# Optimization experiments

Hardware: AMD Instinct MI355X
Metric: run time of the kernel (lower is better)

The kernel has to match this reference:

```python
import jax, jax.numpy as jnp
import numpy as np

NH = 16            # num_heads
HD = 64            # head_dim
HID = NH * HD      # hidden_size = 1024
MLP = 4 * HID      # mlp_hidden_dim = 4096
B, LI, LT = 1, 2048, 512
EPS = 1e-6


def _ln(x):
    # LayerNorm without affine, eps=1e-6
    mu = jnp.mean(x, -1, keepdims=True)
    var = jnp.mean((x - mu) ** 2, -1, keepdims=True)
    return (x - mu) * jax.lax.rsqrt(var + EPS)


def _rms(x, scale):
    # QK RMSNorm over head_dim with learned scale
    return x * jax.lax.rsqrt(jnp.mean(x * x, -1, keepdims=True) + EPS) * scale


def _modulate(vec, w, b):
    # Modulation(double=True): Linear(silu(vec)) -> 6 chunks, broadcast over seq
    out = jnp.dot(jax.nn.silu(vec), w) + b           # [B, 6*HID]
    return jnp.split(out[:, None, :], 6, axis=-1)


def _qkv(x_mod, qkv_w, q_scale, k_scale):
    b, l, _ = x_mod.shape
    qkv = jnp.dot(x_mod, qkv_w).reshape(b, l, 3, NH, HD)
    qkv = jnp.transpose(qkv, (2, 0, 3, 1, 4))         # [3, B, H, L, D]
    q, k, v = qkv[0], qkv[1], qkv[2]
    return _rms(q, q_scale), _rms(k, k_scale), v


def _attn(q, k, v):
    s = jnp.einsum('bhqd,bhkd->bhqk', q, k) * (HD ** -0.5)
    a = jax.nn.softmax(s, axis=-1)
    o = jnp.einsum('bhqk,bhkd->bhqd', a, v)
    b, h, l, d = o.shape
    return jnp.transpose(o, (0, 2, 1, 3)).reshape(b, l, h * d)  # B L (H D)


def _mlp(x, w1, b1, w2, b2):
    return jnp.dot(jax.nn.gelu(jnp.dot(x, w1) + b1, approximate=True), w2) + b2


def setup_inputs() -> dict:
    key = jax.random.key(0)
    ks = iter(jax.random.split(key, 40))
    def rn(shape, s=1.0):
        return jax.random.normal(next(ks), shape, jnp.float32) * s
    return {
        'img': rn((B, LI, HID)),
        'txt': rn((B, LT, HID)),
        'vec': rn((B, HID)),
        'img_mod_w': rn((HID, 6 * HID), 0.02), 'img_mod_b': jnp.zeros((6 * HID,), jnp.float32),
        'txt_mod_w': rn((HID, 6 * HID), 0.02), 'txt_mod_b': jnp.zeros((6 * HID,), jnp.float32),
        'img_qkv_w': rn((HID, 3 * HID), 0.02),
        'img_q_scale': jnp.ones((HD,), jnp.float32), 'img_k_scale': jnp.ones((HD,), jnp.float32),
        'img_proj_w': rn((HID, HID), 0.02), 'img_proj_b': jnp.zeros((HID,), jnp.float32),
        'img_mlp_w1': rn((HID, MLP), 0.02), 'img_mlp_b1': jnp.zeros((MLP,), jnp.float32),
        'img_mlp_w2': rn((MLP, HID), 0.02), 'img_mlp_b2': jnp.zeros((HID,), jnp.float32),
        'txt_qkv_w': rn((HID, 3 * HID), 0.02),
        'txt_q_scale': jnp.ones((HD,), jnp.float32), 'txt_k_scale': jnp.ones((HD,), jnp.float32),
        'txt_proj_w': rn((HID, HID), 0.02), 'txt_proj_b': jnp.zeros((HID,), jnp.float32),
        'txt_mlp_w1': rn((HID, MLP), 0.02), 'txt_mlp_b1': jnp.zeros((MLP,), jnp.float32),
        'txt_mlp_w2': rn((MLP, HID), 0.02), 'txt_mlp_b2': jnp.zeros((HID,), jnp.float32),
    }


def reference(img, txt, vec,
              img_mod_w, img_mod_b, txt_mod_w, txt_mod_b,
              img_qkv_w, img_q_scale, img_k_scale, img_proj_w, img_proj_b,
              img_mlp_w1, img_mlp_b1, img_mlp_w2, img_mlp_b2,
              txt_qkv_w, txt_q_scale, txt_k_scale, txt_proj_w, txt_proj_b,
              txt_mlp_w1, txt_mlp_b1, txt_mlp_w2, txt_mlp_b2):
    i_sh1, i_sc1, i_g1, i_sh2, i_sc2, i_g2 = _modulate(vec, img_mod_w, img_mod_b)
    t_sh1, t_sc1, t_g1, t_sh2, t_sc2, t_g2 = _modulate(vec, txt_mod_w, txt_mod_b)
    iq, ik, iv = _qkv((1 + i_sc1) * _ln(img) + i_sh1, img_qkv_w, img_q_scale, img_k_scale)
    tq, tk, tv = _qkv((1 + t_sc1) * _ln(txt) + t_sh1, txt_qkv_w, txt_q_scale, txt_k_scale)
    q = jnp.concatenate((tq, iq), axis=2)   # txt tokens first, as in source
    k = jnp.concatenate((tk, ik), axis=2)
    v = jnp.concatenate((tv, iv), axis=2)
    attn = _attn(q, k, v)                    # [B, LT+LI, HID]
    lt = txt.shape[1]
    txt_a, img_a = attn[:, :lt], attn[:, lt:]
    img = img + i_g1 * (jnp.dot(img_a, img_proj_w) + img_proj_b)
    img = img + i_g2 * _mlp((1 + i_sc2) * _ln(img) + i_sh2, img_mlp_w1, img_mlp_b1, img_mlp_w2, img_mlp_b2)
    txt = txt + t_g1 * (jnp.dot(txt_a, txt_proj_w) + txt_proj_b)
    txt = txt + t_g2 * _mlp((1 + t_sc2) * _ln(txt) + t_sh2, txt_mlp_w1, txt_mlp_b1, txt_mlp_w2, txt_mlp_b2)
    return (img, txt)
```

## Files before the change

kernel.cpp:

```cpp
#include <hip/hip_runtime.h>
#include <hip/hip_bf16.h>
#include <stdint.h>


#define NHEAD 16
#define HDIM  64
#define HIDD  1024
#define MLPD  4096
#define L_IMG 2048
#define L_TXT 512
#define L_TOT 2560
#define EPSV  1e-6f
#define LOG2E 1.44269504088896f

typedef __attribute__((ext_vector_type(8))) __bf16 bf16x8;
typedef __attribute__((ext_vector_type(4))) float  f32x4;

__device__ __forceinline__ float u2f(uint16_t u) {
    uint32_t i = (uint32_t)u << 16;
    float f; __builtin_memcpy(&f, &i, 4);
    return f;
}
__device__ __forceinline__ uint16_t f2u(float f) {
    uint32_t i; __builtin_memcpy(&i, &f, 4);
    uint32_t r = (i + 0x7fffu + ((i >> 16) & 1u)) >> 16;
    return (uint16_t)r;
}
__device__ __forceinline__ uint32_t pk2(float a, float b) {
    __hip_bfloat162 h = __float22bfloat162_rn(float2{a, b});
    uint32_t r; __builtin_memcpy(&r, &h, 4);
    return r;
}
__device__ __forceinline__ float gelu_tanh(float x) {
    float x3 = x * x * x;
    float t  = tanhf(0.7978845608028654f * (x + 0.044715f * x3));
    return 0.5f * x * (1.f + t);
}

__global__ __launch_bounds__(256) void transpose_f32_bf16(const float* __restrict__ in,
                                                          uint16_t* __restrict__ out,
                                                          int K, int N) {
    __shared__ float tile[64][65];
    const int t  = threadIdx.x;
    const int c0 = blockIdx.x * 64;
    const int r0 = blockIdx.y * 64;
#pragma unroll
    for (int p = 0; p < 4; p++) {
        int row  = p * 16 + (t >> 4);
        int col4 = (t & 15) * 4;
        float4 v = *(const float4*)(in + (size_t)(r0 + row) * N + c0 + col4);
        tile[row][col4 + 0] = v.x; tile[row][col4 + 1] = v.y;
        tile[row][col4 + 2] = v.z; tile[row][col4 + 3] = v.w;
    }
    __syncthreads();
#pragma unroll
    for (int p = 0; p < 4; p++) {
        int row  = p * 16 + (t >> 4);
        int col4 = (t & 15) * 4;
        ushort4 v;
        v.x = f2u(tile[col4 + 0][row]); v.y = f2u(tile[col4 + 1][row]);
        v.z = f2u(tile[col4 + 2][row]); v.w = f2u(tile[col4 + 3][row]);
        *(ushort4*)(out + (size_t)(c0 + row) * K + r0 + col4) = v;
    }
}

__global__ __launch_bounds__(256) void transpose_v_kernel(const uint16_t* __restrict__ Vb,
                                                          uint16_t* __restrict__ Vt) {
    __shared__ uint16_t tile[64][68];
    const int t  = threadIdx.x;
    const int p0 = blockIdx.x * 64;
    const int h  = blockIdx.y;
    const uint16_t* src = Vb + ((size_t)h * L_TOT + p0) * HDIM;
#pragma unroll
    for (int p = 0; p < 4; p++) {
        int row = p * 16 + (t >> 4);
        int c4  = (t & 15) * 4;
        ushort4 v = *(const ushort4*)(src + (size_t)row * HDIM + c4);
        tile[row][c4 + 0] = v.x; tile[row][c4 + 1] = v.y;
        tile[row][c4 + 2] = v.z; tile[row][c4 + 3] = v.w;
    }
    __syncthreads();
    uint16_t* dst = Vt + (size_t)h * HDIM * L_TOT;
#pragma unroll
    for (int p = 0; p < 4; p++) {
        int d  = p * 16 + (t >> 4);
        int c4 = (t & 15) * 4;
        ushort4 v;
        v.x = tile[c4 + 0][d]; v.y = tile[c4 + 1][d];
        v.z = tile[c4 + 2][d]; v.w = tile[c4 + 3][d];
        *(ushort4*)(dst + (size_t)d * L_TOT + p0 + c4) = v;
    }
}

__global__ __launch_bounds__(256) void mod_gemv_kernel(const float* __restrict__ vec,
                                                       const float* __restrict__ w,
                                                       const float* __restrict__ b,
                                                       float* __restrict__ mod) {
    __shared__ float s[HIDD];
    __shared__ float part[4][64];
    const int t = threadIdx.x;
    for (int i = t; i < HIDD; i += 256) {
        float x = vec[i];
        s[i] = x / (1.f + __expf(-x));
    }
    __syncthreads();
    const int col = blockIdx.x * 64 + (t & 63);
    const int ks  = t >> 6;
    float acc = 0.f;
#pragma unroll 8
    for (int k = ks * 256; k < ks * 256 + 256; k++)
        acc += s[k] * w[(size_t)k * 6144 + col];
    part[ks][t & 63] = acc;
    __syncthreads();
    if (t < 64) {
        float r = part[0][t] + part[1][t] + part[2][t] + part[3][t];
        mod[blockIdx.x * 64 + t] = r + b[blockIdx.x * 64 + t];
    }
}

__global__ __launch_bounds__(256) void ln_mod_kernel(const float* __restrict__ x,
                                                     const float* __restrict__ mod,
                                                     int scOff, int shOff,
                                                     uint16_t* __restrict__ xm) {
    __shared__ float red[8];
    const int row = blockIdx.x, t = threadIdx.x;
    const size_t base = (size_t)row * HIDD + t * 4;
    float4 u = *(const float4*)(x + base);
    float v[4] = {u.x, u.y, u.z, u.w};
    float s = v[0] + v[1] + v[2] + v[3];
    float q = v[0]*v[0] + v[1]*v[1] + v[2]*v[2] + v[3]*v[3];
#pragma unroll
    for (int o = 32; o; o >>= 1) { s += __shfl_down(s, o); q += __shfl_down(q, o); }
    if ((t & 63) == 0) { red[t >> 6] = s; red[4 + (t >> 6)] = q; }
    __syncthreads();
    s = red[0] + red[1] + red[2] + red[3];
    q = red[4] + red[5] + red[6] + red[7];
    const float mu  = s * (1.f / HIDD);
    const float var = q * (1.f / HIDD) - mu * mu;
    const float rs  = rsqrtf(var + EPSV);
    ushort4 o;
    {
        int col = t * 4;
        float y0 = (v[0] - mu) * rs, y1 = (v[1] - mu) * rs;
        float y2 = (v[2] - mu) * rs, y3 = (v[3] - mu) * rs;
        o.x = f2u(y0 + mod[scOff + col + 0] * y0 + mod[shOff + col + 0]);
        o.y = f2u(y1 + mod[scOff + col + 1] * y1 + mod[shOff + col + 1]);
        o.z = f2u(y2 + mod[scOff + col + 2] * y2 + mod[shOff + col + 2]);
        o.w = f2u(y3 + mod[scOff + col + 3] * y3 + mod[shOff + col + 3]);
    }
    *(ushort4*)(xm + base) = o;
}

template <int EPI>
__global__ __launch_bounds__(256, 2) void gemm_kernel(
        const uint16_t* __restrict__ A0, const uint16_t* __restrict__ A1,
        const uint16_t* __restrict__ B0, const uint16_t* __restrict__ B1,
        int M0, int M1, int N, int K,
        const float* __restrict__ bias0, const float* __restrict__ bias1,
        const float* __restrict__ gate0, const float* __restrict__ gate1,
        const float* __restrict__ resid0, const float* __restrict__ resid1,
        void* __restrict__ C0, void* __restrict__ C1) {
    const int z = blockIdx.z;
    const int M = z ? M1 : M0;
    const int m0 = blockIdx.y * 128;
    if (m0 >= M) return;
    const uint16_t* A     = z ? A1 : A0;
    const uint16_t* BT    = z ? B1 : B0;
    const float*    bias  = z ? bias1 : bias0;
    const float*    gate  = z ? gate1 : gate0;
    const float*    resid = z ? resid1 : resid0;
    void*           C     = z ? C1 : C0;

    __shared__ uint16_t As[128 * 32];
    __shared__ uint16_t Bs[128 * 32];
    const int t = threadIdx.x;
    const int w = t >> 6, l = t & 63;
    const int lr = l & 15, lg = l >> 4;
    const int n0 = blockIdx.x * 128;
    const int srow = l >> 2, scol = (l & 3) * 8;
    const int c0 = w * 2;
    const int wr = (w >> 1) * 64, wc = (w & 1) * 64;

    const f32x4 z4 = {0.f, 0.f, 0.f, 0.f};
    f32x4 acc[4][4];
#pragma unroll
    for (int i = 0; i < 4; i++)
#pragma unroll
        for (int j = 0; j < 4; j++) acc[i][j] = z4;

    for (int kt = 0; kt < K; kt += 32) {
        __syncthreads();
#pragma unroll
        for (int i = 0; i < 2; i++) {
            const int c = c0 + i;
            const uint16_t* ga = A  + (size_t)(m0 + c * 16 + srow) * K + kt + scol;
            const uint16_t* gb = BT + (size_t)(n0 + c * 16 + srow) * K + kt + scol;
            __builtin_amdgcn_global_load_lds(
                (__attribute__((address_space(1))) void*)ga,
                (__attribute__((address_space(3))) void*)(As + c * 512), 16, 0, 0);
            __builtin_amdgcn_global_load_lds(
                (__attribute__((address_space(1))) void*)gb,
                (__attribute__((address_space(3))) void*)(Bs + c * 512), 16, 0, 0);
        }
        __syncthreads();
        bf16x8 af[4], bfr[4];
#pragma unroll
        for (int mi = 0; mi < 4; mi++)
            af[mi] = *(const bf16x8*)(As + (wr + mi * 16 + lr) * 32 + lg * 8);
#pragma unroll
        for (int nj = 0; nj < 4; nj++)
            bfr[nj] = *(const bf16x8*)(Bs + (wc + nj * 16 + lr) * 32 + lg * 8);
#pragma unroll
        for (int mi = 0; mi < 4; mi++)
#pragma unroll
            for (int nj = 0; nj < 4; nj++)
                acc[mi][nj] = __builtin_amdgcn_mfma_f32_16x16x32_bf16(
                    af[mi], bfr[nj], acc[mi][nj], 0, 0, 0);
    }

#pragma unroll
    for (int mi = 0; mi < 4; mi++)
#pragma unroll
        for (int nj = 0; nj < 4; nj++) {
            const int col = n0 + wc + nj * 16 + lr;
            float bv = 0.f, gv = 0.f;
            if (EPI != 0) bv = bias[col];
            if (EPI == 2) gv = gate[col];
#pragma unroll
            for (int j = 0; j < 4; j++) {
                const int row = m0 + wr + mi * 16 + lg * 4 + j;
                const size_t idx = (size_t)row * N + col;
                float v = acc[mi][nj][j];
                if (EPI == 0) {
                    ((uint16_t*)C)[idx] = f2u(v);
                } else if (EPI == 1) {
                    ((uint16_t*)C)[idx] = f2u(gelu_tanh(v + bv));
                } else {
                    ((float*)C)[idx] = resid[idx] + gv * (v + bv);
                }
            }
        }
}

__global__ __launch_bounds__(256, 2) void gemm_splitk_kernel(
        const uint16_t* __restrict__ A0, const uint16_t* __restrict__ A1,
        const uint16_t* __restrict__ B0, const uint16_t* __restrict__ B1,
        int M0, int M1, int N, int K, int KS,
        float* __restrict__ P0, float* __restrict__ P1) {
    const int z = blockIdx.z & 1;
    const int split = blockIdx.z >> 1;
    const int M = z ? M1 : M0;
    const int m0 = blockIdx.y * 128;
    if (m0 >= M) return;
    const uint16_t* A  = z ? A1 : A0;
    const uint16_t* BT = z ? B1 : B0;
    float* P = (z ? P1 : P0) + (size_t)split * M * N;

    __shared__ uint16_t As[128 * 32];
    __shared__ uint16_t Bs[128 * 32];
    const int t = threadIdx.x;
    const int w = t >> 6, l = t & 63;
    const int lr = l & 15, lg = l >> 4;
    const int n0 = blockIdx.x * 128;
    const int srow = l >> 2, scol = (l & 3) * 8;
    const int c0 = w * 2;
    const int wr = (w >> 1) * 64, wc = (w & 1) * 64;

    const f32x4 z4 = {0.f, 0.f, 0.f, 0.f};
    f32x4 acc[4][4];
#pragma unroll
    for (int i = 0; i < 4; i++)
#pragma unroll
        for (int j = 0; j < 4; j++) acc[i][j] = z4;

    const int kbeg = split * KS, kend = kbeg + KS;
    for (int kt = kbeg; kt < kend; kt += 32) {
        __syncthreads();
#pragma unroll
        for (int i = 0; i < 2; i++) {
            const int c = c0 + i;
            const uint16_t* ga = A  + (size_t)(m0 + c * 16 + srow) * K + kt + scol;
            const uint16_t* gb = BT + (size_t)(n0 + c * 16 + srow) * K + kt + scol;
            __builtin_amdgcn_global_load_lds(
                (__attribute__((address_space(1))) void*)ga,
                (__attribute__((address_space(3))) void*)(As + c * 512), 16, 0, 0);
            __builtin_amdgcn_global_load_lds(
                (__attribute__((address_space(1))) void*)gb,
                (__attribute__((address_space(3))) void*)(Bs + c * 512), 16, 0, 0);
        }
        __syncthreads();
        bf16x8 af[4], bfr[4];
#pragma unroll
        for (int mi = 0; mi < 4; mi++)
            af[mi] = *(const bf16x8*)(As + (wr + mi * 16 + lr) * 32 + lg * 8);
#pragma unroll
        for (int nj = 0; nj < 4; nj++)
            bfr[nj] = *(const bf16x8*)(Bs + (wc + nj * 16 + lr) * 32 + lg * 8);
#pragma unroll
        for (int mi = 0; mi < 4; mi++)
#pragma unroll
            for (int nj = 0; nj < 4; nj++)
                acc[mi][nj] = __builtin_amdgcn_mfma_f32_16x16x32_bf16(
                    af[mi], bfr[nj], acc[mi][nj], 0, 0, 0);
    }

#pragma unroll
    for (int mi = 0; mi < 4; mi++)
#pragma unroll
        for (int nj = 0; nj < 4; nj++) {
            const int col = n0 + wc + nj * 16 + lr;
#pragma unroll
            for (int j = 0; j < 4; j++) {
                const int row = m0 + wr + mi * 16 + lg * 4 + j;
                P[(size_t)row * N + col] = acc[mi][nj][j];
            }
        }
}

__global__ __launch_bounds__(256) void mlp2_reduce_kernel(
        const float* __restrict__ P0, const float* __restrict__ P1,
        const float* __restrict__ bias0, const float* __restrict__ bias1,
        const float* __restrict__ gate0, const float* __restrict__ gate1,
        const float* __restrict__ resid0, const float* __restrict__ resid1,
        float* __restrict__ O0, float* __restrict__ O1, int M0, int M1) {
    const int z = blockIdx.z;
    const float* P     = z ? P1 : P0;
    const float* bias  = z ? bias1 : bias0;
    const float* gate  = z ? gate1 : gate0;
    const float* resid = z ? resid1 : resid0;
    float*       O     = z ? O1 : O0;
    const int M = z ? M1 : M0;
    const size_t MN = (size_t)M * HIDD;
    const size_t nvec = MN / 4;
    for (size_t i = blockIdx.x * 256 + threadIdx.x; i < nvec; i += (size_t)gridDim.x * 256) {
        const size_t e = i * 4;
        const int col = (int)(e & (HIDD - 1));
        float4 a  = *(const float4*)(P + e);
        float4 b  = *(const float4*)(P + MN + e);
        float4 r  = *(const float4*)(resid + e);
        float4 bi = *(const float4*)(bias + col);
        float4 g  = *(const float4*)(gate + col);
        float4 o;
        o.x = r.x + g.x * (a.x + b.x + bi.x);
        o.y = r.y + g.y * (a.y + b.y + bi.y);
        o.z = r.z + g.z * (a.z + b.z + bi.z);
        o.w = r.w + g.w * (a.w + b.w + bi.w);
        *(float4*)(O + e) = o;
    }
}

__global__ __launch_bounds__(256) void rms_scatter_kernel(
        const uint16_t* __restrict__ qkv, int L, int glOff,
        const float* __restrict__ qs, const float* __restrict__ ks,
        uint16_t* __restrict__ Q, uint16_t* __restrict__ Kb, uint16_t* __restrict__ V) {
    const int row = blockIdx.x;
    const int t = threadIdx.x;
    const int head = t >> 4, d0 = (t & 15) * 4;
    const uint16_t* base = qkv + (size_t)row * 3072;
    const size_t obase = ((size_t)head * L_TOT + (glOff + row)) * HDIM + d0;
    {
        ushort4 u = *(const ushort4*)(base + head * HDIM + d0);
        float v0 = u2f(u.x), v1 = u2f(u.y), v2 = u2f(u.z), v3 = u2f(u.w);
        float ss = v0*v0 + v1*v1 + v2*v2 + v3*v3;
        ss += __shfl_xor(ss, 1); ss += __shfl_xor(ss, 2);
        ss += __shfl_xor(ss, 4); ss += __shfl_xor(ss, 8);
        float inv = rsqrtf(ss * (1.f / HDIM) + EPSV) * (0.125f * LOG2E);
        ushort4 o;
        o.x = f2u(v0 * inv * qs[d0 + 0]);
        o.y = f2u(v1 * inv * qs[d0 + 1]);
        o.z = f2u(v2 * inv * qs[d0 + 2]);
        o.w = f2u(v3 * inv * qs[d0 + 3]);
        *(ushort4*)(Q + obase) = o;
    }
    {
        ushort4 u = *(const ushort4*)(base + HIDD + head * HDIM + d0);
        float v0 = u2f(u.x), v1 = u2f(u.y), v2 = u2f(u.z), v3 = u2f(u.w);
        float ss = v0*v0 + v1*v1 + v2*v2 + v3*v3;
        ss += __shfl_xor(ss, 1); ss += __shfl_xor(ss, 2);
        ss += __shfl_xor(ss, 4); ss += __shfl_xor(ss, 8);
        float inv = rsqrtf(ss * (1.f / HDIM) + EPSV);
        ushort4 o;
        o.x = f2u(v0 * inv * ks[d0 + 0]);
        o.y = f2u(v1 * inv * ks[d0 + 1]);
        o.z = f2u(v2 * inv * ks[d0 + 2]);
        o.w = f2u(v3 * inv * ks[d0 + 3]);
        *(ushort4*)(Kb + obase) = o;
    }
    {
        ushort4 u = *(const ushort4*)(base + 2 * HIDD + head * HDIM + d0);
        *(ushort4*)(V + obase) = u;
    }
}

__global__ __launch_bounds__(256, 4) void attn_kernel(const uint16_t* __restrict__ Q,
                                                      const uint16_t* __restrict__ Kg,
                                                      const uint16_t* __restrict__ Vt,
                                                      uint16_t* __restrict__ Opart,
                                                      float* __restrict__ ml) {
    __shared__ __align__(16) uint16_t Ks[64 * 64];
    __shared__ __align__(16) uint16_t Vs[64 * 64];
    __shared__ __align__(16) uint16_t Pl[4][16][72];
    const int t = threadIdx.x;
    const int w = t >> 6, l = t & 63;
    const int lr = l & 15, lg = l >> 4;
    const int h = blockIdx.y;
    const int s = blockIdx.z;
    const int q0 = blockIdx.x * 64 + w * 16;
    const uint16_t* Qh = Q  + (size_t)h * L_TOT * HDIM;
    const uint16_t* Kh = Kg + (size_t)h * L_TOT * HDIM;
    const uint16_t* Vh = Vt + (size_t)h * HDIM * L_TOT;

    const bf16x8 qf0 = *(const bf16x8*)(Qh + (size_t)(q0 + lr) * HDIM + lg * 8);
    const bf16x8 qf1 = *(const bf16x8*)(Qh + (size_t)(q0 + lr) * HDIM + 32 + lg * 8);

    const int rl = l >> 3;
    const int ce = ((l & 7) ^ rl) * 8;
    const int r0 = w * 16 + rl;
    const int r1 = r0 + 8;
    const int sw = lr & 7;

    const f32x4 z4 = {0.f, 0.f, 0.f, 0.f};
    f32x4 of[4] = {z4, z4, z4, z4};
    float m = -1e30f, lsum = 0.f;

    const int kbeg = s * (L_TOT / 2);
    for (int it = 0; it < (L_TOT / 2) / 64; ++it) {
        const int k0 = kbeg + it * 64;
        __syncthreads();
        __builtin_amdgcn_global_load_lds(
            (__attribute__((address_space(1))) void*)(Kh + (size_t)(k0 + r0) * HDIM + ce),
            (__attribute__((address_space(3))) void*)(Ks + w * 1024), 16, 0, 0);
        __builtin_amdgcn_global_load_lds(
            (__attribute__((address_space(1))) void*)(Kh + (size_t)(k0 + r1) * HDIM + ce),
            (__attribute__((address_space(3))) void*)(Ks + w * 1024 + 512), 16, 0, 0);
        __builtin_amdgcn_global_load_lds(
            (__attribute__((address_space(1))) void*)(Vh + (size_t)r0 * L_TOT + k0 + ce),
            (__attribute__((address_space(3))) void*)(Vs + w * 1024), 16, 0, 0);
        __builtin_amdgcn_global_load_lds(
            (__attribute__((address_space(1))) void*)(Vh + (size_t)r1 * L_TOT + k0 + ce),
            (__attribute__((address_space(3))) void*)(Vs + w * 1024 + 512), 16, 0, 0);
        __syncthreads();
        f32x4 sf[4] = {z4, z4, z4, z4};
#pragma unroll
        for (int kb = 0; kb < 4; kb++) {
            bf16x8 a0 = *(const bf16x8*)(Ks + (kb * 16 + lr) * 64 + ((lg ^ sw) * 8));
            bf16x8 a1 = *(const bf16x8*)(Ks + (kb * 16 + lr) * 64 + (((4 + lg) ^ sw) * 8));
            sf[kb] = __builtin_amdgcn_mfma_f32_16x16x32_bf16(a0, qf0, sf[kb], 0, 0, 0);
            sf[kb] = __builtin_amdgcn_mfma_f32_16x16x32_bf16(a1, qf1, sf[kb], 0, 0, 0);
        }
        float mt = sf[0][0];
#pragma unroll
        for (int kb = 0; kb < 4; kb++)
#pragma unroll
            for (int j = 0; j < 4; j++) mt = fmaxf(mt, sf[kb][j]);
        mt = fmaxf(mt, __shfl_xor(mt, 16));
        mt = fmaxf(mt, __shfl_xor(mt, 32));
        if (__any(mt > m)) {
            float mn = fmaxf(m, mt);
            float c  = exp2f(m - mn);
            m = mn; lsum *= c;
#pragma unroll
            for (int dj = 0; dj < 4; dj++)
#pragma unroll
                for (int j = 0; j < 4; j++) of[dj][j] *= c;
        }
        uint32_t pw[8];
        float rs = 0.f;
#pragma unroll
        for (int kb = 0; kb < 4; kb++) {
            float p0 = exp2f(sf[kb][0] - m);
            float p1 = exp2f(sf[kb][1] - m);
            float p2 = exp2f(sf[kb][2] - m);
            float p3 = exp2f(sf[kb][3] - m);
            rs += (p0 + p1) + (p2 + p3);
            pw[kb * 2]     = pk2(p0, p1);
            pw[kb * 2 + 1] = pk2(p2, p3);
        }
        lsum += rs;
#pragma unroll
        for (int kb = 0; kb < 4; kb++) {
            uint2 u = {pw[kb * 2], pw[kb * 2 + 1]};
            *(uint2*)&Pl[w][lr][kb * 16 + lg * 4] = u;
        }
        bf16x8 pb0 = *(const bf16x8*)&Pl[w][lr][lg * 8];
        bf16x8 pb1 = *(const bf16x8*)&Pl[w][lr][32 + lg * 8];
#pragma unroll
        for (int dj = 0; dj < 4; dj++) {
            bf16x8 v0 = *(const bf16x8*)(Vs + (dj * 16 + lr) * 64 + ((lg ^ sw) * 8));
            bf16x8 v1 = *(const bf16x8*)(Vs + (dj * 16 + lr) * 64 + (((4 + lg) ^ sw) * 8));
            of[dj] = __builtin_amdgcn_mfma_f32_16x16x32_bf16(v0, pb0, of[dj], 0, 0, 0);
            of[dj] = __builtin_amdgcn_mfma_f32_16x16x32_bf16(v1, pb1, of[dj], 0, 0, 0);
        }
    }
    lsum += __shfl_xor(lsum, 16);
    lsum += __shfl_xor(lsum, 32);
    const float inv = 1.f / lsum;
    const int row = q0 + lr;
    const size_t ob = ((size_t)(s * NHEAD + h) * L_TOT + row) * HDIM;
#pragma unroll
    for (int dj = 0; dj < 4; dj++) {
        uint2 u;
        u.x = pk2(of[dj][0] * inv, of[dj][1] * inv);
        u.y = pk2(of[dj][2] * inv, of[dj][3] * inv);
        *(uint2*)(Opart + ob + dj * 16 + lg * 4) = u;
    }
    if (lg == 0) {
        const size_t mb = ((size_t)(s * NHEAD + h) * L_TOT + row) * 2;
        ml[mb]     = m;
        ml[mb + 1] = lsum;
    }
}

__global__ __launch_bounds__(256) void attn_merge_kernel(const uint16_t* __restrict__ Opart,
                                                         const float* __restrict__ ml,
                                                         uint16_t* __restrict__ attn) {
    const int t = threadIdx.x;
    const int row = blockIdx.x * 16 + (t >> 4);
    const int h = blockIdx.y;
    const int d = (t & 15) * 4;
    const size_t i0 = (size_t)(0 * NHEAD + h) * L_TOT + row;
    const size_t i1 = (size_t)(1 * NHEAD + h) * L_TOT + row;
    float m0 = ml[i0 * 2], l0 = ml[i0 * 2 + 1];
    float m1 = ml[i1 * 2], l1 = ml[i1 * 2 + 1];
    float mM = fmaxf(m0, m1);
    float w0 = l0 * exp2f(m0 - mM);
    float w1 = l1 * exp2f(m1 - mM);
    float inv = 1.f / (w0 + w1);
    w0 *= inv; w1 *= inv;
    ushort4 a = *(const ushort4*)(Opart + i0 * HDIM + d);
    ushort4 b = *(const ushort4*)(Opart + i1 * HDIM + d);
    ushort4 o;
    o.x = f2u(u2f(a.x) * w0 + u2f(b.x) * w1);
    o.y = f2u(u2f(a.y) * w0 + u2f(b.y) * w1);
    o.z = f2u(u2f(a.z) * w0 + u2f(b.z) * w1);
    o.w = f2u(u2f(a.w) * w0 + u2f(b.w) * w1);
    *(ushort4*)(attn + (size_t)row * HIDD + h * HDIM + d) = o;
}

extern "C" void kernel_launch(void* const* d_in, const int* in_sizes, int n_in,
                              void* d_out, int out_size, void* d_ws, size_t ws_size,
                              hipStream_t stream) {
    const float* img        = (const float*)d_in[0];
    const float* txt        = (const float*)d_in[1];
    const float* vec        = (const float*)d_in[2];
    const float* img_mod_w  = (const float*)d_in[3];
    const float* img_mod_b  = (const float*)d_in[4];
    const float* txt_mod_w  = (const float*)d_in[5];
    const float* txt_mod_b  = (const float*)d_in[6];
    const float* img_qkv_w  = (const float*)d_in[7];
    const float* img_q_s    = (const float*)d_in[8];
    const float* img_k_s    = (const float*)d_in[9];
    const float* img_proj_w = (const float*)d_in[10];
    const float* img_proj_b = (const float*)d_in[11];
    const float* img_mlp_w1 = (const float*)d_in[12];
    const float* img_mlp_b1 = (const float*)d_in[13];
    const float* img_mlp_w2 = (const float*)d_in[14];
    const float* img_mlp_b2 = (const float*)d_in[15];
    const float* txt_qkv_w  = (const float*)d_in[16];
    const float* txt_q_s    = (const float*)d_in[17];
    const float* txt_k_s    = (const float*)d_in[18];
    const float* txt_proj_w = (const float*)d_in[19];
    const float* txt_proj_b = (const float*)d_in[20];
    const float* txt_mlp_w1 = (const float*)d_in[21];
    const float* txt_mlp_b1 = (const float*)d_in[22];
    const float* txt_mlp_w2 = (const float*)d_in[23];
    const float* txt_mlp_b2 = (const float*)d_in[24];

    float* out_img = (float*)d_out;
    float* out_txt = out_img + (size_t)L_IMG * HIDD;

    char* ws = (char*)d_ws;
    size_t off = 0;
    auto alloc = [&](size_t bytes) -> void* {
        void* p = ws + off;
        off += bytes;
        off = (off + 255) & ~(size_t)255;
        return p;
    };
    uint16_t* wtQKVi = (uint16_t*)alloc((size_t)3072 * 1024 * 2);
    uint16_t* wtQKVt = (uint16_t*)alloc((size_t)3072 * 1024 * 2);
    uint16_t* wtPRJi = (uint16_t*)alloc((size_t)1024 * 1024 * 2);
    uint16_t* wtPRJt = (uint16_t*)alloc((size_t)1024 * 1024 * 2);
    uint16_t* wtM1i  = (uint16_t*)alloc((size_t)4096 * 1024 * 2);
    uint16_t* wtM1t  = (uint16_t*)alloc((size_t)4096 * 1024 * 2);
    uint16_t* wtM2i  = (uint16_t*)alloc((size_t)1024 * 4096 * 2);
    uint16_t* wtM2t  = (uint16_t*)alloc((size_t)1024 * 4096 * 2);
    float*    modi   = (float*)alloc(6144 * 4);
    float*    modt   = (float*)alloc(6144 * 4);
    uint16_t* xm1i   = (uint16_t*)alloc((size_t)L_IMG * HIDD * 2);
    uint16_t* xm1t   = (uint16_t*)alloc((size_t)L_TXT * HIDD * 2);
    uint16_t* qkvi   = (uint16_t*)alloc((size_t)L_IMG * 3072 * 2);
    uint16_t* qkvt   = (uint16_t*)alloc((size_t)L_TXT * 3072 * 2);
    uint16_t* Qb     = (uint16_t*)alloc((size_t)NHEAD * L_TOT * HDIM * 2);
    uint16_t* Kb     = (uint16_t*)alloc((size_t)NHEAD * L_TOT * HDIM * 2);
    uint16_t* Vb     = (uint16_t*)alloc((size_t)NHEAD * L_TOT * HDIM * 2);
    uint16_t* Vtb    = (uint16_t*)alloc((size_t)NHEAD * L_TOT * HDIM * 2);
    uint16_t* attn   = (uint16_t*)alloc((size_t)L_TOT * HIDD * 2);
    float*    x2i    = (float*)alloc((size_t)L_IMG * HIDD * 4);
    float*    x2t    = (float*)alloc((size_t)L_TXT * HIDD * 4);
    uint16_t* xm2i   = (uint16_t*)alloc((size_t)L_IMG * HIDD * 2);
    uint16_t* xm2t   = (uint16_t*)alloc((size_t)L_TXT * HIDD * 2);
    uint16_t* hi     = (uint16_t*)alloc((size_t)L_IMG * MLPD * 2);
    uint16_t* ht     = (uint16_t*)alloc((size_t)L_TXT * MLPD * 2);
    uint16_t* Opart  = qkvi;
    float*    mlbuf  = (float*)qkvt;
    float*    pM2i   = (float*)Qb;
    float*    pM2t   = pM2i + (size_t)2 * L_IMG * HIDD;
    (void)ws_size; (void)in_sizes; (void)n_in; (void)out_size;

    transpose_f32_bf16<<<dim3(3072 / 64, 1024 / 64), 256, 0, stream>>>(img_qkv_w, wtQKVi, 1024, 3072);
    transpose_f32_bf16<<<dim3(3072 / 64, 1024 / 64), 256, 0, stream>>>(txt_qkv_w, wtQKVt, 1024, 3072);
    transpose_f32_bf16<<<dim3(1024 / 64, 1024 / 64), 256, 0, stream>>>(img_proj_w, wtPRJi, 1024, 1024);
    transpose_f32_bf16<<<dim3(1024 / 64, 1024 / 64), 256, 0, stream>>>(txt_proj_w, wtPRJt, 1024, 1024);
    transpose_f32_bf16<<<dim3(4096 / 64, 1024 / 64), 256, 0, stream>>>(img_mlp_w1, wtM1i, 1024, 4096);
    transpose_f32_bf16<<<dim3(4096 / 64, 1024 / 64), 256, 0, stream>>>(txt_mlp_w1, wtM1t, 1024, 4096);
    transpose_f32_bf16<<<dim3(1024 / 64, 4096 / 64), 256, 0, stream>>>(img_mlp_w2, wtM2i, 4096, 1024);
    transpose_f32_bf16<<<dim3(1024 / 64, 4096 / 64), 256, 0, stream>>>(txt_mlp_w2, wtM2t, 4096, 1024);

    mod_gemv_kernel<<<96, 256, 0, stream>>>(vec, img_mod_w, img_mod_b, modi);
    mod_gemv_kernel<<<96, 256, 0, stream>>>(vec, txt_mod_w, txt_mod_b, modt);

    ln_mod_kernel<<<L_IMG, 256, 0, stream>>>(img, modi, 1024, 0, xm1i);
    ln_mod_kernel<<<L_TXT, 256, 0, stream>>>(txt, modt, 1024, 0, xm1t);

    gemm_kernel<0><<<dim3(3072 / 128, L_IMG / 128, 2), 256, 0, stream>>>(
        xm1i, xm1t, wtQKVi, wtQKVt, L_IMG, L_TXT, 3072, 1024,
        nullptr, nullptr, nullptr, nullptr, nullptr, nullptr, qkvi, qkvt);

    rms_scatter_kernel<<<L_IMG, 256, 0, stream>>>(qkvi, L_IMG, L_TXT, img_q_s, img_k_s, Qb, Kb, Vb);
    rms_scatter_kernel<<<L_TXT, 256, 0, stream>>>(qkvt, L_TXT, 0, txt_q_s, txt_k_s, Qb, Kb, Vb);

    transpose_v_kernel<<<dim3(L_TOT / 64, NHEAD), 256, 0, stream>>>(Vb, Vtb);

    attn_kernel<<<dim3(L_TOT / 64, NHEAD, 2), 256, 0, stream>>>(Qb, Kb, Vtb, Opart, mlbuf);
    attn_merge_kernel<<<dim3(L_TOT / 16, NHEAD), 256, 0, stream>>>(Opart, mlbuf, attn);

    gemm_kernel<2><<<dim3(1024 / 128, L_IMG / 128, 2), 256, 0, stream>>>(
        attn + (size_t)L_TXT * HIDD, attn, wtPRJi, wtPRJt, L_IMG, L_TXT, 1024, 1024,
        img_proj_b, txt_proj_b, modi + 2048, modt + 2048, img, txt, x2i, x2t);

    ln_mod_kernel<<<L_IMG, 256, 0, stream>>>(x2i, modi, 4096, 3072, xm2i);
    ln_mod_kernel<<<L_TXT, 256, 0, stream>>>(x2t, modt, 4096, 3072, xm2t);

    gemm_kernel<1><<<dim3(MLPD / 128, L_IMG / 128, 2), 256, 0, stream>>>(
        xm2i, xm2t, wtM1i, wtM1t, L_IMG, L_TXT, MLPD, 1024,
        img_mlp_b1, txt_mlp_b1, nullptr, nullptr, nullptr, nullptr, hi, ht);

    gemm_splitk_kernel<<<dim3(1024 / 128, L_IMG / 128, 4), 256, 0, stream>>>(
        hi, ht, wtM2i, wtM2t, L_IMG, L_TXT, 1024, MLPD, MLPD / 2, pM2i, pM2t);
    mlp2_reduce_kernel<<<dim3(512, 1, 2), 256, 0, stream>>>(
        pM2i, pM2t, img_mlp_b2, txt_mlp_b2, modi + 5120, modt + 5120,
        x2i, x2t, out_img, out_txt, L_IMG, L_TXT);
}
```

Before: 322.9 us.

## Double-buffer GEMM LDS, widen attention KV tile, merge launches, split-K projection

The GEMM and split-K GEMM kernels now double-buffer their LDS tiles, so the next K-slice load is issued before the MFMAs on the current slice run. The attention kernel processes 128 keys per iteration instead of 64, using a swizzled V layout, and its occupancy hint drops from 4 to 3. The eight weight transposes, two modulation GEMVs, paired LayerNorm launches and RMS scatter launches are each merged into single launches to cut launch overhead. The output projection switches to split-K with a separate reduce kernel, which adds extra partial-sum traffic.

```diff
diff --git a/kernel.cpp b/kernel.cpp
--- a/kernel.cpp
+++ b/kernel.cpp
@@ -37,13 +37,29 @@
     return 0.5f * x * (1.f + t);
 }
 
-__global__ __launch_bounds__(256) void transpose_f32_bf16(const float* __restrict__ in,
-                                                          uint16_t* __restrict__ out,
-                                                          int K, int N) {
+__global__ __launch_bounds__(256) void transpose_all_kernel(
+        const float* __restrict__ i0, const float* __restrict__ i1,
+        const float* __restrict__ i2, const float* __restrict__ i3,
+        const float* __restrict__ i4, const float* __restrict__ i5,
+        const float* __restrict__ i6, const float* __restrict__ i7,
+        uint16_t* __restrict__ o0, uint16_t* __restrict__ o1,
+        uint16_t* __restrict__ o2, uint16_t* __restrict__ o3,
+        uint16_t* __restrict__ o4, uint16_t* __restrict__ o5,
+        uint16_t* __restrict__ o6, uint16_t* __restrict__ o7) {
     __shared__ float tile[64][65];
-    const int t  = threadIdx.x;
-    const int c0 = blockIdx.x * 64;
-    const int r0 = blockIdx.y * 64;
+    const int b = blockIdx.x, t = threadIdx.x;
+    const float* in; uint16_t* out; int K, N, rel;
+    if      (b < 768)  { in = i0; out = o0; K = 1024; N = 3072; rel = b; }
+    else if (b < 1536) { in = i1; out = o1; K = 1024; N = 3072; rel = b - 768; }
+    else if (b < 1792) { in = i2; out = o2; K = 1024; N = 1024; rel = b - 1536; }
+    else if (b < 2048) { in = i3; out = o3; K = 1024; N = 1024; rel = b - 1792; }
+    else if (b < 3072) { in = i4; out = o4; K = 1024; N = 4096; rel = b - 2048; }
+    else if (b < 4096) { in = i5; out = o5; K = 1024; N = 4096; rel = b - 3072; }
+    else if (b < 5120) { in = i6; out = o6; K = 4096; N = 1024; rel = b - 4096; }
+    else               { in = i7; out = o7; K = 4096; N = 1024; rel = b - 5120; }
+    const int nx = N >> 6;
+    const int c0 = (rel % nx) * 64;
+    const int r0 = (rel / nx) * 64;
 #pragma unroll
     for (int p = 0; p < 4; p++) {
         int row  = p * 16 + (t >> 4);
@@ -93,9 +109,15 @@
 }
 
 __global__ __launch_bounds__(256) void mod_gemv_kernel(const float* __restrict__ vec,
-                                                       const float* __restrict__ w,
-                                                       const float* __restrict__ b,
-                                                       float* __restrict__ mod) {
+                                                       const float* __restrict__ w0,
+                                                       const float* __restrict__ b0,
+                                                       float* __restrict__ m0,
+                                                       const float* __restrict__ w1,
+                                                       const float* __restrict__ b1,
+                                                       float* __restrict__ m1) {
+    const float* w   = blockIdx.z ? w1 : w0;
+    const float* b   = blockIdx.z ? b1 : b0;
+    float*       mod = blockIdx.z ? m1 : m0;
     __shared__ float s[HIDD];
     __shared__ float part[4][64];
     const int t = threadIdx.x;
@@ -118,12 +140,19 @@
     }
 }
 
-__global__ __launch_bounds__(256) void ln_mod_kernel(const float* __restrict__ x,
-                                                     const float* __restrict__ mod,
+__global__ __launch_bounds__(256) void ln_mod_kernel(const float* __restrict__ xi,
+                                                     const float* __restrict__ xt,
+                                                     const float* __restrict__ mi,
+                                                     const float* __restrict__ mt_,
                                                      int scOff, int shOff,
-                                                     uint16_t* __restrict__ xm) {
+                                                     uint16_t* __restrict__ oi,
+                                                     uint16_t* __restrict__ ot) {
     __shared__ float red[8];
-    const int row = blockIdx.x, t = threadIdx.x;
+    int row = blockIdx.x;
+    const float* x; const float* mod; uint16_t* xm;
+    if (row < L_IMG) { x = xi; mod = mi; xm = oi; }
+    else             { x = xt; mod = mt_; xm = ot; row -= L_IMG; }
+    const int t = threadIdx.x;
     const size_t base = (size_t)row * HIDD + t * 4;
     float4 u = *(const float4*)(x + base);
     float v[4] = {u.x, u.y, u.z, u.w};
@@ -171,8 +200,8 @@
     const float*    resid = z ? resid1 : resid0;
     void*           C     = z ? C1 : C0;
 
-    __shared__ uint16_t As[128 * 32];
-    __shared__ uint16_t Bs[128 * 32];
+    __shared__ uint16_t As[2][128 * 32];
+    __shared__ uint16_t Bs[2][128 * 32];
     const int t = threadIdx.x;
     const int w = t >> 6, l = t & 63;
     const int lr = l & 15, lg = l >> 4;
@@ -181,15 +210,7 @@
     const int c0 = w * 2;
     const int wr = (w >> 1) * 64, wc = (w & 1) * 64;
 
-    const f32x4 z4 = {0.f, 0.f, 0.f, 0.f};
-    f32x4 acc[4][4];
-#pragma unroll
-    for (int i = 0; i < 4; i++)
-#pragma unroll
-        for (int j = 0; j < 4; j++) acc[i][j] = z4;
-
-    for (int kt = 0; kt < K; kt += 32) {
-        __syncthreads();
+    auto stage = [&](int buf, int kt) {
 #pragma unroll
         for (int i = 0; i < 2; i++) {
             const int c = c0 + i;
@@ -197,25 +218,39 @@
             const uint16_t* gb = BT + (size_t)(n0 + c * 16 + srow) * K + kt + scol;
             __builtin_amdgcn_global_load_lds(
                 (__attribute__((address_space(1))) void*)ga,
-                (__attribute__((address_space(3))) void*)(As + c * 512), 16, 0, 0);
+                (__attribute__((address_space(3))) void*)(As[buf] + c * 512), 16, 0, 0);
             __builtin_amdgcn_global_load_lds(
                 (__attribute__((address_space(1))) void*)gb,
-                (__attribute__((address_space(3))) void*)(Bs + c * 512), 16, 0, 0);
-        }
+                (__attribute__((address_space(3))) void*)(Bs[buf] + c * 512), 16, 0, 0);
+        }
+    };
+
+    const f32x4 z4 = {0.f, 0.f, 0.f, 0.f};
+    f32x4 acc[4][4];
+#pragma unroll
+    for (int i = 0; i < 4; i++)
+#pragma unroll
+        for (int j = 0; j < 4; j++) acc[i][j] = z4;
+
+    stage(0, 0);
+    int cur = 0;
+    for (int kt = 0; kt < K; kt += 32) {
         __syncthreads();
+        if (kt + 32 < K) stage(cur ^ 1, kt + 32);
         bf16x8 af[4], bfr[4];
 #pragma unroll
         for (int mi = 0; mi < 4; mi++)
-            af[mi] = *(const bf16x8*)(As + (wr + mi * 16 + lr) * 32 + lg * 8);
+            af[mi] = *(const bf16x8*)(As[cur] + (wr + mi * 16 + lr) * 32 + lg * 8);
 #pragma unroll
         for (int nj = 0; nj < 4; nj++)
-            bfr[nj] = *(const bf16x8*)(Bs + (wc + nj * 16 + lr) * 32 + lg * 8);
+            bfr[nj] = *(const bf16x8*)(Bs[cur] + (wc + nj * 16 + lr) * 32 + lg * 8);
 #pragma unroll
         for (int mi = 0; mi < 4; mi++)
 #pragma unroll
             for (int nj = 0; nj < 4; nj++)
                 acc[mi][nj] = __builtin_amdgcn_mfma_f32_16x16x32_bf16(
                     af[mi], bfr[nj], acc[mi][nj], 0, 0, 0);
+        cur ^= 1;
     }
 
 #pragma unroll
@@ -256,8 +291,8 @@
     const uint16_t* BT = z ? B1 : B0;
     float* P = (z ? P1 : P0) + (size_t)split * M * N;
 
-    __shared__ uint16_t As[128 * 32];
-    __shared__ uint16_t Bs[128 * 32];
+    __shared__ uint16_t As[2][128 * 32];
+    __shared__ uint16_t Bs[2][128 * 32];
     const int t = threadIdx.x;
     const int w = t >> 6, l = t & 63;
     const int lr = l & 15, lg = l >> 4;
@@ -266,16 +301,7 @@
     const int c0 = w * 2;
     const int wr = (w >> 1) * 64, wc = (w & 1) * 64;
 
-    const f32x4 z4 = {0.f, 0.f, 0.f, 0.f};
-    f32x4 acc[4][4];
-#pragma unroll
-    for (int i = 0; i < 4; i++)
-#pragma unroll
-        for (int j = 0; j < 4; j++) acc[i][j] = z4;
-
-    const int kbeg = split * KS, kend = kbeg + KS;
-    for (int kt = kbeg; kt < kend; kt += 32) {
-        __syncthreads();
+    auto stage = [&](int buf, int kt) {
 #pragma unroll
         for (int i = 0; i < 2; i++) {
             const int c = c0 + i;
@@ -283,25 +309,40 @@
             const uint16_t* gb = BT + (size_t)(n0 + c * 16 + srow) * K + kt + scol;
             __builtin_amdgcn_global_load_lds(
                 (__attribute__((address_space(1))) void*)ga,
-                (__attribute__((address_space(3))) void*)(As + c * 512), 16, 0, 0);
+                (__attribute__((address_space(3))) void*)(As[buf] + c * 512), 16, 0, 0);
             __builtin_amdgcn_global_load_lds(
                 (__attribute__((address_space(1))) void*)gb,
-                (__attribute__((address_space(3))) void*)(Bs + c * 512), 16, 0, 0);
-        }
+                (__attribute__((address_space(3))) void*)(Bs[buf] + c * 512), 16, 0, 0);
+        }
+    };
+
+    const f32x4 z4 = {0.f, 0.f, 0.f, 0.f};
+    f32x4 acc[4][4];
+#pragma unroll
+    for (int i = 0; i < 4; i++)
+#pragma unroll
+        for (int j = 0; j < 4; j++) acc[i][j] = z4;
+
+    const int kbeg = split * KS, kend = kbeg + KS;
+    stage(0, kbeg);
+    int cur = 0;
+    for (int kt = kbeg; kt < kend; kt += 32) {
         __syncthreads();
+        if (kt + 32 < kend) stage(cur ^ 1, kt + 32);
         bf16x8 af[4], bfr[4];
 #pragma unroll
         for (int mi = 0; mi < 4; mi++)
-            af[mi] = *(const bf16x8*)(As + (wr + mi * 16 + lr) * 32 + lg * 8);
+            af[mi] = *(const bf16x8*)(As[cur] + (wr + mi * 16 + lr) * 32 + lg * 8);
 #pragma unroll
         for (int nj = 0; nj < 4; nj++)
-            bfr[nj] = *(const bf16x8*)(Bs + (wc + nj * 16 + lr) * 32 + lg * 8);
+            bfr[nj] = *(const bf16x8*)(Bs[cur] + (wc + nj * 16 + lr) * 32 + lg * 8);
 #pragma unroll
         for (int mi = 0; mi < 4; mi++)
 #pragma unroll
             for (int nj = 0; nj < 4; nj++)
                 acc[mi][nj] = __builtin_amdgcn_mfma_f32_16x16x32_bf16(
                     af[mi], bfr[nj], acc[mi][nj], 0, 0, 0);
+        cur ^= 1;
     }
 
 #pragma unroll
@@ -317,7 +358,7 @@
         }
 }
 
-__global__ __launch_bounds__(256) void mlp2_reduce_kernel(
+__global__ __launch_bounds__(256) void splitk_reduce_kernel(
         const float* __restrict__ P0, const float* __restrict__ P1,
         const float* __restrict__ bias0, const float* __restrict__ bias1,
         const float* __restrict__ gate0, const float* __restrict__ gate1,
@@ -350,14 +391,18 @@
 }
 
 __global__ __launch_bounds__(256) void rms_scatter_kernel(
-        const uint16_t* __restrict__ qkv, int L, int glOff,
-        const float* __restrict__ qs, const float* __restrict__ ks,
+        const uint16_t* __restrict__ qkvi, const uint16_t* __restrict__ qkvt,
+        const float* __restrict__ iqs, const float* __restrict__ iks,
+        const float* __restrict__ tqs, const float* __restrict__ tks,
         uint16_t* __restrict__ Q, uint16_t* __restrict__ Kb, uint16_t* __restrict__ V) {
-    const int row = blockIdx.x;
+    const int p = blockIdx.x;
+    const uint16_t* base;
+    const float* qs; const float* ks;
+    if (p < L_TXT) { base = qkvt + (size_t)p * 3072;            qs = tqs; ks = tks; }
+    else           { base = qkvi + (size_t)(p - L_TXT) * 3072;  qs = iqs; ks = iks; }
     const int t = threadIdx.x;
     const int head = t >> 4, d0 = (t & 15) * 4;
-    const uint16_t* base = qkv + (size_t)row * 3072;
-    const size_t obase = ((size_t)head * L_TOT + (glOff + row)) * HDIM + d0;
+    const size_t obase = ((size_t)head * L_TOT + p) * HDIM + d0;
     {
         ushort4 u = *(const ushort4*)(base + head * HDIM + d0);
         float v0 = u2f(u.x), v1 = u2f(u.y), v2 = u2f(u.z), v3 = u2f(u.w);
@@ -392,14 +437,15 @@
     }
 }
 
-__global__ __launch_bounds__(256, 4) void attn_kernel(const uint16_t* __restrict__ Q,
+#define KVB 128
+__global__ __launch_bounds__(256, 3) void attn_kernel(const uint16_t* __restrict__ Q,
                                                       const uint16_t* __restrict__ Kg,
                                                       const uint16_t* __restrict__ Vt,
                                                       uint16_t* __restrict__ Opart,
                                                       float* __restrict__ ml) {
-    __shared__ __align__(16) uint16_t Ks[64 * 64];
-    __shared__ __align__(16) uint16_t Vs[64 * 64];
-    __shared__ __align__(16) uint16_t Pl[4][16][72];
+    __shared__ __align__(16) uint16_t Ks[KVB * 64];
+    __shared__ __align__(16) uint16_t Vs[64 * KVB];
+    __shared__ __align__(16) uint16_t Pl[4][16][136];
     const int t = threadIdx.x;
     const int w = t >> 6, l = t & 63;
     const int lr = l & 15, lg = l >> 4;
@@ -413,44 +459,48 @@
     const bf16x8 qf0 = *(const bf16x8*)(Qh + (size_t)(q0 + lr) * HDIM + lg * 8);
     const bf16x8 qf1 = *(const bf16x8*)(Qh + (size_t)(q0 + lr) * HDIM + 32 + lg * 8);
 
-    const int rl = l >> 3;
-    const int ce = ((l & 7) ^ rl) * 8;
-    const int r0 = w * 16 + rl;
-    const int r1 = r0 + 8;
-    const int sw = lr & 7;
+    const int krl = l >> 3;
+    const int kce = ((l & 7) ^ krl) * 8;
+    const int vr0 = l >> 4;
+    const int vsl = l & 15;
+    const int sw  = lr & 7;
 
     const f32x4 z4 = {0.f, 0.f, 0.f, 0.f};
     f32x4 of[4] = {z4, z4, z4, z4};
     float m = -1e30f, lsum = 0.f;
 
     const int kbeg = s * (L_TOT / 2);
-    for (int it = 0; it < (L_TOT / 2) / 64; ++it) {
-        const int k0 = kbeg + it * 64;
+    for (int it = 0; it < (L_TOT / 2) / KVB; ++it) {
+        const int k0 = kbeg + it * KVB;
         __syncthreads();
-        __builtin_amdgcn_global_load_lds(
-            (__attribute__((address_space(1))) void*)(Kh + (size_t)(k0 + r0) * HDIM + ce),
-            (__attribute__((address_space(3))) void*)(Ks + w * 1024), 16, 0, 0);
-        __builtin_amdgcn_global_load_lds(
-            (__attribute__((address_space(1))) void*)(Kh + (size_t)(k0 + r1) * HDIM + ce),
-            (__attribute__((address_space(3))) void*)(Ks + w * 1024 + 512), 16, 0, 0);
-        __builtin_amdgcn_global_load_lds(
-            (__attribute__((address_space(1))) void*)(Vh + (size_t)r0 * L_TOT + k0 + ce),
-            (__attribute__((address_space(3))) void*)(Vs + w * 1024), 16, 0, 0);
-        __builtin_amdgcn_global_load_lds(
-            (__attribute__((address_space(1))) void*)(Vh + (size_t)r1 * L_TOT + k0 + ce),
-            (__attribute__((address_space(3))) void*)(Vs + w * 1024 + 512), 16, 0, 0);
+#pragma unroll
+        for (int i = 0; i < 4; i++) {
+            const int kr = w * 32 + i * 8 + krl;
+            __builtin_amdgcn_global_load_lds(
+                (__attribute__((address_space(1))) void*)(Kh + (size_t)(k0 + kr) * HDIM + kce),
+                (__attribute__((address_space(3))) void*)(Ks + w * 2048 + i * 512), 16, 0, 0);
+        }
+#pragma unroll
+        for (int i = 0; i < 4; i++) {
+            const int vr = w * 16 + i * 4 + vr0;
+            __builtin_amdgcn_global_load_lds(
+                (__attribute__((address_space(1))) void*)(Vh + (size_t)vr * L_TOT + k0 + ((vsl ^ (vr & 7)) * 8)),
+                (__attribute__((address_space(3))) void*)(Vs + w * 2048 + i * 512), 16, 0, 0);
+        }
         __syncthreads();
-        f32x4 sf[4] = {z4, z4, z4, z4};
-#pragma unroll
-        for (int kb = 0; kb < 4; kb++) {
-            bf16x8 a0 = *(const bf16x8*)(Ks + (kb * 16 + lr) * 64 + ((lg ^ sw) * 8));
-            bf16x8 a1 = *(const bf16x8*)(Ks + (kb * 16 + lr) * 64 + (((4 + lg) ^ sw) * 8));
+        f32x4 sf[8];
+#pragma unroll
+        for (int kb = 0; kb < 8; kb++) {
+            sf[kb] = z4;
+            const uint16_t* kr = Ks + (kb * 16 + lr) * 64;
+            bf16x8 a0 = *(const bf16x8*)(kr + ((lg ^ sw) * 8));
+            bf16x8 a1 = *(const bf16x8*)(kr + (((4 + lg) ^ sw) * 8));
             sf[kb] = __builtin_amdgcn_mfma_f32_16x16x32_bf16(a0, qf0, sf[kb], 0, 0, 0);
             sf[kb] = __builtin_amdgcn_mfma_f32_16x16x32_bf16(a1, qf1, sf[kb], 0, 0, 0);
         }
         float mt = sf[0][0];
 #pragma unroll
-        for (int kb = 0; kb < 4; kb++)
+        for (int kb = 0; kb < 8; kb++)
 #pragma unroll
             for (int j = 0; j < 4; j++) mt = fmaxf(mt, sf[kb][j]);
         mt = fmaxf(mt, __shfl_xor(mt, 16));
@@ -464,10 +514,10 @@
 #pragma unroll
                 for (int j = 0; j < 4; j++) of[dj][j] *= c;
         }
-        uint32_t pw[8];
+        uint32_t pw[16];
         float rs = 0.f;
 #pragma unroll
-        for (int kb = 0; kb < 4; kb++) {
+        for (int kb = 0; kb < 8; kb++) {
             float p0 = exp2f(sf[kb][0] - m);
             float p1 = exp2f(sf[kb][1] - m);
             float p2 = exp2f(sf[kb][2] - m);
@@ -478,18 +528,19 @@
         }
         lsum += rs;
 #pragma unroll
-        for (int kb = 0; kb < 4; kb++) {
+        for (int kb = 0; kb < 8; kb++) {
             uint2 u = {pw[kb * 2], pw[kb * 2 + 1]};
             *(uint2*)&Pl[w][lr][kb * 16 + lg * 4] = u;
         }
-        bf16x8 pb0 = *(const bf16x8*)&Pl[w][lr][lg * 8];
-        bf16x8 pb1 = *(const bf16x8*)&Pl[w][lr][32 + lg * 8];
-#pragma unroll
-        for (int dj = 0; dj < 4; dj++) {
-            bf16x8 v0 = *(const bf16x8*)(Vs + (dj * 16 + lr) * 64 + ((lg ^ sw) * 8));
-            bf16x8 v1 = *(const bf16x8*)(Vs + (dj * 16 + lr) * 64 + (((4 + lg) ^ sw) * 8));
-            of[dj] = __builtin_amdgcn_mfma_f32_16x16x32_bf16(v0, pb0, of[dj], 0, 0, 0);
-            of[dj] = __builtin_amdgcn_mfma_f32_16x16x32_bf16(v1, pb1, of[dj], 0, 0, 0);
+#pragma unroll
+        for (int ks = 0; ks < 4; ks++) {
+            bf16x8 pb = *(const bf16x8*)&Pl[w][lr][ks * 32 + lg * 8];
+#pragma unroll
+            for (int dj = 0; dj < 4; dj++) {
+                const uint16_t* vrp = Vs + (dj * 16 + lr) * KVB;
+                bf16x8 vv = *(const bf16x8*)(vrp + (((ks * 4 + lg) ^ sw) * 8));
+                of[dj] = __builtin_amdgcn_mfma_f32_16x16x32_bf16(vv, pb, of[dj], 0, 0, 0);
+            }
         }
     }
     lsum += __shfl_xor(lsum, 16);
@@ -604,51 +655,48 @@
     uint16_t* ht     = (uint16_t*)alloc((size_t)L_TXT * MLPD * 2);
     uint16_t* Opart  = qkvi;
     float*    mlbuf  = (float*)qkvt;
-    float*    pM2i   = (float*)Qb;
-    float*    pM2t   = pM2i + (size_t)2 * L_IMG * HIDD;
+    float*    pSKi   = (float*)Qb;
+    float*    pSKt   = pSKi + (size_t)2 * L_IMG * HIDD;
     (void)ws_size; (void)in_sizes; (void)n_in; (void)out_size;
 
-    transpose_f32_bf16<<<dim3(3072 / 64, 1024 / 64), 256, 0, stream>>>(img_qkv_w, wtQKVi, 1024, 3072);
-    transpose_f32_bf16<<<dim3(3072 / 64, 1024 / 64), 256, 0, stream>>>(txt_qkv_w, wtQKVt, 1024, 3072);
-    transpose_f32_bf16<<<dim3(1024 / 64, 1024 / 64), 256, 0, stream>>>(img_proj_w, wtPRJi, 1024, 1024);
-    transpose_f32_bf16<<<dim3(1024 / 64, 1024 / 64), 256, 0, stream>>>(txt_proj_w, wtPRJt, 1024, 1024);
-    transpose_f32_bf16<<<dim3(4096 / 64, 1024 / 64), 256, 0, stream>>>(img_mlp_w1, wtM1i, 1024, 4096);
-    transpose_f32_bf16<<<dim3(4096 / 64, 1024 / 64), 256, 0, stream>>>(txt_mlp_w1, wtM1t, 1024, 4096);
-    transpose_f32_bf16<<<dim3(1024 / 64, 4096 / 64), 256, 0, stream>>>(img_mlp_w2, wtM2i, 4096, 1024);
-    transpose_f32_bf16<<<dim3(1024 / 64, 4096 / 64), 256, 0, stream>>>(txt_mlp_w2, wtM2t, 4096, 1024);
-
-    mod_gemv_kernel<<<96, 256, 0, stream>>>(vec, img_mod_w, img_mod_b, modi);
-    mod_gemv_kernel<<<96, 256, 0, stream>>>(vec, txt_mod_w, txt_mod_b, modt);
-
-    ln_mod_kernel<<<L_IMG, 256, 0, stream>>>(img, modi, 1024, 0, xm1i);
-    ln_mod_kernel<<<L_TXT, 256, 0, stream>>>(txt, modt, 1024, 0, xm1t);
+    transpose_all_kernel<<<6144, 256, 0, stream>>>(
+        img_qkv_w, txt_qkv_w, img_proj_w, txt_proj_w,
+        img_mlp_w1, txt_mlp_w1, img_mlp_w2, txt_mlp_w2,
+        wtQKVi, wtQKVt, wtPRJi, wtPRJt, wtM1i, wtM1t, wtM2i, wtM2t);
+
+    mod_gemv_kernel<<<dim3(96, 1, 2), 256, 0, stream>>>(
+        vec, img_mod_w, img_mod_b, modi, txt_mod_w, txt_mod_b, modt);
+
+    ln_mod_kernel<<<L_IMG + L_TXT, 256, 0, stream>>>(img, txt, modi, modt, 1024, 0, xm1i, xm1t);
 
     gemm_kernel<0><<<dim3(3072 / 128, L_IMG / 128, 2), 256, 0, stream>>>(
         xm1i, xm1t, wtQKVi, wtQKVt, L_IMG, L_TXT, 3072, 1024,
         nullptr, nullptr, nullptr, nullptr, nullptr, nullptr, qkvi, qkvt);
 
-    rms_scatter_kernel<<<L_IMG, 256, 0, stream>>>(qkvi, L_IMG, L_TXT, img_q_s, img_k_s, Qb, Kb, Vb);
-    rms_scatter_kernel<<<L_TXT, 256, 0, stream>>>(qkvt, L_TXT, 0, txt_q_s, txt_k_s, Qb, Kb, Vb);
+    rms_scatter_kernel<<<L_TOT, 256, 0, stream>>>(
+        qkvi, qkvt, img_q_s, img_k_s, txt_q_s, txt_k_s, Qb, Kb, Vb);
 
     transpose_v_kernel<<<dim3(L_TOT / 64, NHEAD), 256, 0, stream>>>(Vb, Vtb);
 
     attn_kernel<<<dim3(L_TOT / 64, NHEAD, 2), 256, 0, stream>>>(Qb, Kb, Vtb, Opart, mlbuf);
     attn_merge_kernel<<<dim3(L_TOT / 16, NHEAD), 256, 0, stream>>>(Opart, mlbuf, attn);
 
-    gemm_kernel<2><<<dim3(1024 / 128, L_IMG / 128, 2), 256, 0, stream>>>(
-        attn + (size_t)L_TXT * HIDD, attn, wtPRJi, wtPRJt, L_IMG, L_TXT, 1024, 1024,
-        img_proj_b, txt_proj_b, modi + 2048, modt + 2048, img, txt, x2i, x2t);
-
-    ln_mod_kernel<<<L_IMG, 256, 0, stream>>>(x2i, modi, 4096, 3072, xm2i);
-    ln_mod_kernel<<<L_TXT, 256, 0, stream>>>(x2t, modt, 4096, 3072, xm2t);
+    gemm_splitk_kernel<<<dim3(1024 / 128, L_IMG / 128, 4), 256, 0, stream>>>(
+        attn + (size_t)L_TXT * HIDD, attn, wtPRJi, wtPRJt, L_IMG, L_TXT, 1024, 1024, 512,
+        pSKi, pSKt);
+    splitk_reduce_kernel<<<dim3(512, 1, 2), 256, 0, stream>>>(
+        pSKi, pSKt, img_proj_b, txt_proj_b, modi + 2048, modt + 2048,
+        img, txt, x2i, x2t, L_IMG, L_TXT);
+
+    ln_mod_kernel<<<L_IMG + L_TXT, 256, 0, stream>>>(x2i, x2t, modi, modt, 4096, 3072, xm2i, xm2t);
 
     gemm_kernel<1><<<dim3(MLPD / 128, L_IMG / 128, 2), 256, 0, stream>>>(
         xm2i, xm2t, wtM1i, wtM1t, L_IMG, L_TXT, MLPD, 1024,
         img_mlp_b1, txt_mlp_b1, nullptr, nullptr, nullptr, nullptr, hi, ht);
 
     gemm_splitk_kernel<<<dim3(1024 / 128, L_IMG / 128, 4), 256, 0, stream>>>(
-        hi, ht, wtM2i, wtM2t, L_IMG, L_TXT, 1024, MLPD, MLPD / 2, pM2i, pM2t);
-    mlp2_reduce_kernel<<<dim3(512, 1, 2), 256, 0, stream>>>(
-        pM2i, pM2t, img_mlp_b2, txt_mlp_b2, modi + 5120, modt + 5120,
+        hi, ht, wtM2i, wtM2t, L_IMG, L_TXT, 1024, MLPD, MLPD / 2, pSKi, pSKt);
+    splitk_reduce_kernel<<<dim3(512, 1, 2), 256, 0, stream>>>(
+        pSKi, pSKt, img_mlp_b2, txt_mlp_b2, modi + 5120, modt + 5120,
         x2i, x2t, out_img, out_txt, L_IMG, L_TXT);
 }
```

After: 285.8 us. 11.5% less time.
